# Performance work log

Measured on AMD Instinct MI355X. Metric: run time of the kernel, lower is better.

## Reference

```python
import jax, jax.numpy as jnp
import numpy as np

B, C, N, V, W = 2, 4, 224, 7, 256
EMB, H = 256, 4
TOKEN_DIM = C * N           # 896
HF = int(C * 2.66)          # 10 (GDFN hidden features)
EPS_LN = 1e-6


def _dwconv3(x, w):
    # depthwise 3x3, padding=1; x:[B,Ch,Hh,Ww], w:[Ch,1,3,3]
    return jax.lax.conv_general_dilated(
        x, w, window_strides=(1, 1), padding='SAME',
        feature_group_count=x.shape[1],
        dimension_numbers=('NCHW', 'OIHW', 'NCHW'))


def _layernorm_c(x, g, b):
    # LayerNorm over channel dim (NCHW), eps=1e-6
    m = jnp.mean(x, axis=1, keepdims=True)
    v = jnp.mean((x - m) ** 2, axis=1, keepdims=True)
    return (x - m) / jnp.sqrt(v + EPS_LN) * g[None, :, None, None] + b[None, :, None, None]


def setup_inputs() -> dict:
    key = jax.random.key(0)
    ks = jax.random.split(key, 12)
    s = 0.02
    return {
        'buffer':     jax.random.normal(ks[0], (B, C, N, V, W), jnp.float32),
        'w_in':       jax.random.normal(ks[1], (EMB, TOKEN_DIM), jnp.float32) * s,
        'temperature': jnp.ones((1, H, 1, 1), jnp.float32),
        'ln1_g':      jnp.ones((EMB,), jnp.float32),
        'ln1_b':      jnp.zeros((EMB,), jnp.float32),
        'w_qkv':      jax.random.normal(ks[2], (3 * EMB, EMB), jnp.float32) * s,
        'w_qkv_dw':   jax.random.normal(ks[3], (3 * EMB, 1, 3, 3), jnp.float32) * s,
        'w_proj':     jax.random.normal(ks[4], (TOKEN_DIM, EMB), jnp.float32) * s,
        'w_attca':    jax.random.normal(ks[5], (2 * H, H), jnp.float32) * s,
        'ln2_g':      jnp.ones((C,), jnp.float32),
        'ln2_b':      jnp.zeros((C,), jnp.float32),
        'w_pin':      jax.random.normal(ks[6], (2 * HF, C), jnp.float32) * s,
        'w_dw':       jax.random.normal(ks[7], (2 * HF, 1, 3, 3), jnp.float32) * s,
        'w_pout':     jax.random.normal(ks[8], (C, HF), jnp.float32) * s,
    }


def reference(buffer, w_in, temperature, ln1_g, ln1_b, w_qkv, w_qkv_dw,
              w_proj, w_attca, ln2_g, ln2_b, w_pin, w_dw, w_pout):
    S = V * W
    d = EMB // H
    # b c n v w -> b (v w) (c n)
    x_tok = buffer.transpose(0, 3, 4, 1, 2).reshape(B, S, C * N)
    # b c n v w -> (b n) c v w
    x_res = buffer.transpose(0, 2, 1, 3, 4).reshape(B * N, C, V, W)

    x_tok = jnp.einsum('bsk,ek->bse', x_tok, w_in)                  # linear_in
    x = x_tok.reshape(B, V, W, EMB).transpose(0, 3, 1, 2)           # b emb v w
    x_norm = _layernorm_c(x, ln1_g, ln1_b)

    qkv = jnp.einsum('bchw,oc->bohw', x_norm, w_qkv)                # 1x1 conv
    qkv = _dwconv3(qkv, w_qkv_dw)
    q, k, v_ = jnp.split(qkv, 3, axis=1)

    def heads(t):  # b (h d) v w -> b h (v w) d
        return t.reshape(B, H, d, S).transpose(0, 1, 3, 2)
    q, k, v_ = heads(q), heads(k), heads(v_)

    # F.normalize(dim=-1), eps=1e-12
    q = q / jnp.maximum(jnp.linalg.norm(q, axis=-1, keepdims=True), 1e-12)
    k = k / jnp.maximum(jnp.linalg.norm(k, axis=-1, keepdims=True), 1e-12)

    attn_logits = jnp.einsum('bhid,bhjd->bhij', q, k) * temperature
    attn0 = jax.nn.softmax(attn_logits, axis=-1)
    attn1 = jnp.maximum(attn_logits, 0.0) ** 2
    attn1 = jax.nn.gelu(attn1, approximate=False) * attn1
    x_att = jnp.einsum('bhij,oh->boij', attn1, w_attca)             # 1x1 conv over heads
    scale, shift = jnp.split(x_att, 2, axis=1)
    attn = attn0 * (1.0 + scale) + shift

    out = jnp.einsum('bhij,bhjd->bhid', attn, v_)
    out = out.transpose(0, 1, 3, 2).reshape(B, EMB, V, W)           # b (h d) v w
    out = jnp.einsum('bchw,oc->bohw', out, w_proj)                  # proj to token_dim
    out = out.reshape(B, C, N, V, W).transpose(0, 2, 1, 3, 4).reshape(B * N, C, V, W)

    x2 = x_res + out
    epi = _layernorm_c(x2, ln2_g, ln2_b)
    # GDFN
    h_ = jnp.einsum('bchw,oc->bohw', epi, w_pin)
    h_ = _dwconv3(h_, w_dw)
    h1, h2 = jnp.split(h_, 2, axis=1)
    h_ = jax.nn.gelu(h1, approximate=False) * h2
    epi = jnp.einsum('bchw,oc->bohw', h_, w_pout)
    epi = x2 + epi

    return epi.reshape(B, N, C, V, W).transpose(0, 2, 1, 3, 4)      # b c n v w
```

## Files before the change

kernel.cpp:

```cpp
#include <hip/hip_runtime.h>
#include <math.h>

#define B_ 2
#define C_ 4
#define N_ 224
#define V_ 7
#define W_ 256
#define S_ 1792
#define EMB_ 256
#define H_ 4
#define D_ 64
#define TOK_ 896
#define HF_ 10
#define JC_ 4
#define JRANGE_ (S_ / JC_)
#define JSTEPS_ (JRANGE_ / 32)

typedef __attribute__((ext_vector_type(8))) short short8;
typedef __attribute__((ext_vector_type(4))) float f32x4;

#define MFMA16(a, b, c) __builtin_amdgcn_mfma_f32_16x16x32_bf16(a, b, c, 0, 0, 0)

__device__ inline short f2bf(float f) {
    union { float f; unsigned u; } x; x.f = f;
    unsigned u = x.u;
    unsigned r = (u + 0x7fffu + ((u >> 16) & 1u)) >> 16;
    return (short)r;
}
__device__ inline float bf2f(short s) {
    union { unsigned u; float f; } x;
    x.u = ((unsigned)(unsigned short)s) << 16;
    return x.f;
}

template<bool COLSUM, bool LNB, bool BBF>
__global__ __launch_bounds__(256) void gemm_kernel(
    const float* __restrict__ A, const void* __restrict__ Bv, float* __restrict__ Cm,
    int M, int N, int K, long b_bs, long c_bs,
    const float* __restrict__ csin, float* __restrict__ csout,
    const float* __restrict__ lg, const float* __restrict__ lb)
{
    const int bz = blockIdx.z;
    Cm += (long)bz * c_bs;
    const int m0 = blockIdx.y * 64, n0 = blockIdx.x * 128;
    __shared__ __align__(16) short As[64 * 32];
    __shared__ __align__(16) short Bs[128 * 32];
    const int t = threadIdx.x;
    const int lane = t & 63, wave = t >> 6;
    const int wr = wave >> 1, wc = wave & 1;
    const int col = lane & 15, grp = lane >> 4;
    const int arow = t >> 2, akc = (t & 3) * 8;
    const int bn = t & 127, bkc = (t >> 7) * 16;
    float mean = 0.f, rstd = 1.f;
    if (LNB) {
        float s = 0.f, q = 0.f;
        #pragma unroll
        for (int mb = 0; mb < 4; ++mb) {
            s += csin[((long)(bz * 4 + mb) * 2 + 0) * N + n0 + bn];
            q += csin[((long)(bz * 4 + mb) * 2 + 1) * N + n0 + bn];
        }
        mean = s * (1.f / 256.f);
        rstd = rsqrtf(q * (1.f / 256.f) - mean * mean + 1e-6f);
    }
    f32x4 acc[2][4];
    #pragma unroll
    for (int i = 0; i < 2; ++i)
        #pragma unroll
        for (int j = 0; j < 4; ++j) acc[i][j] = (f32x4){0.f, 0.f, 0.f, 0.f};
    for (int k0 = 0; k0 < K; k0 += 32) {
        {
            const float* ap = &A[(long)(m0 + arow) * K + k0 + akc];
            f32x4 a0 = *(const f32x4*)ap;
            f32x4 a1 = *(const f32x4*)(ap + 4);
            short8 av;
            av[0] = f2bf(a0[0]); av[1] = f2bf(a0[1]); av[2] = f2bf(a0[2]); av[3] = f2bf(a0[3]);
            av[4] = f2bf(a1[0]); av[5] = f2bf(a1[1]); av[6] = f2bf(a1[2]); av[7] = f2bf(a1[3]);
            int abyte = (arow << 6) + (akc << 1);
            *(short8*)((char*)As + (abyte ^ ((arow & 7) << 4))) = av;
        }
        {
            short8 b0, b1;
            if (BBF) {
                const short* Bp = (const short*)Bv + (long)bz * b_bs;
                #pragma unroll
                for (int j = 0; j < 8; ++j) {
                    b0[j] = Bp[(long)(k0 + bkc + j) * N + n0 + bn];
                    b1[j] = Bp[(long)(k0 + bkc + 8 + j) * N + n0 + bn];
                }
            } else {
                const float* Bp = (const float*)Bv + (long)bz * b_bs;
                #pragma unroll
                for (int j = 0; j < 16; ++j) {
                    float v = Bp[(long)(k0 + bkc + j) * N + n0 + bn];
                    if (LNB) v = fmaf((v - mean) * rstd, lg[k0 + bkc + j], lb[k0 + bkc + j]);
                    if (j < 8) b0[j] = f2bf(v); else b1[j - 8] = f2bf(v);
                }
            }
            int bbyte = (bn << 6) + (bkc << 1);
            *(short8*)((char*)Bs + ((bbyte) ^ ((bn & 7) << 4))) = b0;
            *(short8*)((char*)Bs + ((bbyte + 16) ^ ((bn & 7) << 4))) = b1;
        }
        __syncthreads();
        short8 af[2], bfv[4];
        #pragma unroll
        for (int mm = 0; mm < 2; ++mm) {
            int r = wr * 32 + mm * 16 + col;
            af[mm] = *(const short8*)((const char*)As + (((r << 6) + (grp << 4)) ^ ((r & 7) << 4)));
        }
        #pragma unroll
        for (int nn = 0; nn < 4; ++nn) {
            int r = wc * 64 + nn * 16 + col;
            bfv[nn] = *(const short8*)((const char*)Bs + (((r << 6) + (grp << 4)) ^ ((r & 7) << 4)));
        }
        #pragma unroll
        for (int mm = 0; mm < 2; ++mm)
            #pragma unroll
            for (int nn = 0; nn < 4; ++nn)
                acc[mm][nn] = MFMA16(af[mm], bfv[nn], acc[mm][nn]);
        __syncthreads();
    }
    #pragma unroll
    for (int mm = 0; mm < 2; ++mm)
        #pragma unroll
        for (int nn = 0; nn < 4; ++nn)
            #pragma unroll
            for (int r = 0; r < 4; ++r)
                Cm[(long)(m0 + wr * 32 + mm * 16 + grp * 4 + r) * N
                   + n0 + wc * 64 + nn * 16 + col] = acc[mm][nn][r];
    if (COLSUM) {
        float* red = (float*)As;
        #pragma unroll
        for (int nn = 0; nn < 4; ++nn) {
            float s = 0.f, q = 0.f;
            #pragma unroll
            for (int mm = 0; mm < 2; ++mm)
                #pragma unroll
                for (int r = 0; r < 4; ++r) { float v = acc[mm][nn][r]; s += v; q += v * v; }
            s += __shfl_xor(s, 16, 64); s += __shfl_xor(s, 32, 64);
            q += __shfl_xor(q, 16, 64); q += __shfl_xor(q, 32, 64);
            if (lane < 16) {
                int cidx = wc * 64 + nn * 16 + col;
                red[(wr * 128 + cidx) * 2]     = s;
                red[(wr * 128 + cidx) * 2 + 1] = q;
            }
        }
        __syncthreads();
        if (wave < 2 && lane < 16) {
            #pragma unroll
            for (int nn = 0; nn < 4; ++nn) {
                int cidx = wc * 64 + nn * 16 + col;
                float s = red[cidx * 2]     + red[(128 + cidx) * 2];
                float q = red[cidx * 2 + 1] + red[(128 + cidx) * 2 + 1];
                csout[((long)(bz * 4 + blockIdx.y) * 2 + 0) * N + n0 + cidx] = s;
                csout[((long)(bz * 4 + blockIdx.y) * 2 + 1) * N + n0 + cidx] = q;
            }
        }
    }
}

__global__ void dwconv3_kernel(const float* __restrict__ X, const float* __restrict__ Wt,
                               float* __restrict__ Y, short* __restrict__ vbf,
                               long total, int Ch)
{
    long idx = (long)blockIdx.x * blockDim.x + threadIdx.x;
    long stride = (long)gridDim.x * blockDim.x;
    for (; idx < total; idx += stride) {
        int w = (int)(idx % W_);
        long t = idx / W_;
        int h = (int)(t % V_); t /= V_;
        int ch = (int)(t % Ch);
        long img_ch = idx / ((long)V_ * W_);
        const float* wp = Wt + ch * 9;
        const float* xp = X + img_ch * (V_ * W_);
        float acc = 0.f;
        #pragma unroll
        for (int dy = -1; dy <= 1; ++dy) {
            int h2 = h + dy;
            if (h2 < 0 || h2 >= V_) continue;
            #pragma unroll
            for (int dx = -1; dx <= 1; ++dx) {
                int w2 = w + dx;
                if (w2 < 0 || w2 >= W_) continue;
                acc += xp[h2 * W_ + w2] * wp[(dy + 1) * 3 + (dx + 1)];
            }
        }
        Y[idx] = acc;
        if (vbf && ch >= 512) {
            int b = (int)(t / Ch);
            vbf[((long)b * 256 + (ch - 512)) * S_ + h * W_ + w] = f2bf(acc);
        }
    }
}

__global__ __launch_bounds__(256) void headnorm_kernel(
    const float* __restrict__ qkvd, const float* __restrict__ temp,
    short* __restrict__ qn, short* __restrict__ kn)
{
    int s0 = blockIdx.x * 64;
    int bh = blockIdx.y; int b = bh >> 2, h = bh & 3;
    int isq = blockIdx.z;
    int ch0 = b * 768 + (isq ? 0 : EMB_) + h * 64;
    short* dst = (isq ? qn : kn) + (long)bh * S_ * 64;
    __shared__ float tile[64][65];
    __shared__ float red[64][4];
    int t = threadIdx.x;
    int sl = t & 63, dg = t >> 6;
    float part = 0.f;
    for (int dd = 0; dd < 16; ++dd) {
        int d = dg * 16 + dd;
        float v = qkvd[(long)(ch0 + d) * S_ + s0 + sl];
        tile[sl][d] = v;
        part += v * v;
    }
    red[sl][dg] = part;
    __syncthreads();
    int d = t & 63, sg = t >> 6;
    float tmul = isq ? temp[h] : 1.f;
    for (int si = 0; si < 16; ++si) {
        int s = sg * 16 + si;
        float nrm = sqrtf(red[s][0] + red[s][1] + red[s][2] + red[s][3]);
        float scale = tmul / fmaxf(nrm, 1e-12f);
        dst[(long)(s0 + s) * 64 + d] = f2bf(tile[s][d] * scale);
    }
}

__global__ __launch_bounds__(256) void attn_kernel(
    const short* __restrict__ qn, const short* __restrict__ kn,
    const short* __restrict__ vbf, const float* __restrict__ wat,
    short* __restrict__ partY, float* __restrict__ partZ)
{
    const int h = threadIdx.x >> 6;
    const int lane = threadIdx.x & 63;
    const int col = lane & 15, grp = lane >> 4;
    const int itile = blockIdx.x;
    const int jc = blockIdx.y;
    const int b = blockIdx.z;
    const int ibase = itile * 16;
    const int bh = b * 4 + h;

    const short* qrow = qn + ((long)bh * S_ + ibase + col) * 64 + grp * 8;
    short8 qa0 = *(const short8*)qrow;
    short8 qa1 = *(const short8*)(qrow + 32);
    float wsc[4], wsh[4];
    #pragma unroll
    for (int hh = 0; hh < 4; ++hh) { wsc[hh] = wat[h * 4 + hh]; wsh[hh] = wat[(4 + h) * 4 + hh]; }

    __shared__ __align__(16) float exch[2][4][16][36];

    f32x4 y1[4], y2[4];
    #pragma unroll
    for (int dt = 0; dt < 4; ++dt) {
        y1[dt] = (f32x4){0.f, 0.f, 0.f, 0.f};
        y2[dt] = (f32x4){0.f, 0.f, 0.f, 0.f};
    }
    float z = 0.f;
    const short* kbase = kn + (long)bh * S_ * 64;
    const short* vbase = vbf + ((long)b * 256 + h * 64) * S_;
    const int joffA = (col & 3) + 8 * (col >> 2);

    for (int jt = 0; jt < JSTEPS_; ++jt) {
        const int jbase = jc * JRANGE_ + jt * 32;
        const int buf = jt & 1;
        f32x4 lf[2];
        __builtin_amdgcn_s_setprio(1);
        #pragma unroll
        for (int tt = 0; tt < 2; ++tt) {
            const short* krow = kbase + (long)(jbase + joffA + 4 * tt) * 64 + grp * 8;
            short8 ka0 = *(const short8*)krow;
            short8 ka1 = *(const short8*)(krow + 32);
            f32x4 a = (f32x4){0.f, 0.f, 0.f, 0.f};
            a = MFMA16(ka0, qa0, a);
            a = MFMA16(ka1, qa1, a);
            lf[tt] = a;
        }
        __builtin_amdgcn_s_setprio(0);
        f32x4 a1v[2];
        float ee[2][4];
        #pragma unroll
        for (int tt = 0; tt < 2; ++tt) {
            #pragma unroll
            for (int r = 0; r < 4; ++r) {
                float l = lf[tt][r];
                float rr = fmaxf(l, 0.f);
                float s1 = rr * rr;
                float u = fmaf(s1 * s1, 0.0713548162726f * s1, 1.59576912161f * s1);
                float sg = __builtin_amdgcn_rcpf(1.f + __expf(-u));
                a1v[tt][r] = s1 * sg * s1;
                ee[tt][r] = __expf(l);
            }
            *(f32x4*)&exch[buf][h][col][8 * grp + 4 * tt] = a1v[tt];
        }
        __syncthreads();
        short8 pa, pb;
        #pragma unroll
        for (int tt = 0; tt < 2; ++tt) {
            f32x4 scv = a1v[tt] * wsc[h];
            f32x4 shv = a1v[tt] * wsh[h];
            #pragma unroll
            for (int hh = 0; hh < 4; ++hh) {
                if (hh == h) continue;
                f32x4 o = *(const f32x4*)&exch[buf][hh][col][8 * grp + 4 * tt];
                scv += o * wsc[hh];
                shv += o * wsh[hh];
            }
            #pragma unroll
            for (int r = 0; r < 4; ++r) {
                float e = ee[tt][r];
                z += e;
                pa[tt * 4 + r] = f2bf(e * (1.f + scv[r]));
                pb[tt * 4 + r] = f2bf(shv[r]);
            }
        }
        __builtin_amdgcn_s_setprio(1);
        #pragma unroll
        for (int dt = 0; dt < 4; ++dt) {
            const short* vrow = vbase + (long)(dt * 16 + col) * S_ + jbase + grp * 8;
            short8 vb = *(const short8*)vrow;
            y1[dt] = MFMA16(pa, vb, y1[dt]);
            y2[dt] = MFMA16(pb, vb, y2[dt]);
        }
        __builtin_amdgcn_s_setprio(0);
    }

    z += __shfl_xor(z, 16, 64);
    z += __shfl_xor(z, 32, 64);
    if (grp == 0)
        partZ[((long)(jc * 2 + b) * 4 + h) * S_ + ibase + col] = z;

    float* tb = &exch[0][h][0][0];
    long ybase = ((((long)jc * 2 + b) * 4 + h) * 2) * 64 * S_;
    for (int acc = 0; acc < 2; ++acc) {
        #pragma unroll
        for (int dt = 0; dt < 4; ++dt) {
            f32x4 y = acc ? y2[dt] : y1[dt];
            #pragma unroll
            for (int r = 0; r < 4; ++r) tb[(grp * 4 + r) * 17 + col] = y[r];
            #pragma unroll
            for (int p = 0; p < 4; ++p) {
                float val = tb[col * 17 + p * 4 + grp];
                partY[ybase + ((long)acc * 64 + dt * 16 + p * 4 + grp) * S_ + ibase + col] = f2bf(val);
            }
        }
    }
}

__global__ __launch_bounds__(256) void combine_kernel(
    const short* __restrict__ partY, const float* __restrict__ partZ,
    short* __restrict__ outav)
{
    int idx = blockIdx.x * 256 + threadIdx.x;
    int i = idx % S_;
    int t = idx / S_;
    int d = t & 63; t >>= 6;
    int h = t & 3; int b = t >> 2;
    float y1 = 0.f, y2 = 0.f, z = 0.f;
    #pragma unroll
    for (int jc = 0; jc < JC_; ++jc) {
        long base = ((((long)jc * 2 + b) * 4 + h) * 2) * 64 * S_;
        y1 += bf2f(partY[base + (long)d * S_ + i]);
        y2 += bf2f(partY[base + (long)(64 + d) * S_ + i]);
        z  += partZ[((long)(jc * 2 + b) * 4 + h) * S_ + i];
    }
    outav[((long)b * 256 + h * 64 + d) * S_ + i] = f2bf(y1 / z + y2);
}

__global__ __launch_bounds__(256) void resid_pin_kernel(
    const float* __restrict__ buffer, const float* __restrict__ proj,
    const float* __restrict__ g2, const float* __restrict__ b2,
    const float* __restrict__ w_pin,
    float* __restrict__ x2, short* __restrict__ hbuf)
{
    int s = blockIdx.x * 256 + threadIdx.x;
    int bn = blockIdx.y;
    int b = bn / N_, n = bn % N_;
    float v[4];
    float sum = 0.f;
    #pragma unroll
    for (int c = 0; c < 4; ++c) {
        float xr = buffer[((long)(b * 4 + c) * N_ + n) * S_ + s];
        float pr = proj[((long)b * TOK_ + c * N_ + n) * S_ + s];
        v[c] = xr + pr;
        x2[((long)bn * 4 + c) * S_ + s] = v[c];
        sum += v[c];
    }
    float mean = sum * 0.25f;
    float var = 0.f;
    #pragma unroll
    for (int c = 0; c < 4; ++c) { float dd = v[c] - mean; var += dd * dd; }
    var *= 0.25f;
    float inv = rsqrtf(var + 1e-6f);
    float e[4];
    #pragma unroll
    for (int c = 0; c < 4; ++c) e[c] = (v[c] - mean) * inv * g2[c] + b2[c];
    for (int o = 0; o < 2 * HF_; ++o) {
        float a = 0.f;
        #pragma unroll
        for (int c = 0; c < 4; ++c) a += w_pin[o * 4 + c] * e[c];
        hbuf[((long)bn * (2 * HF_) + o) * S_ + s] = f2bf(a);
    }
}

__global__ __launch_bounds__(448) void gdfn_kernel(
    const short* __restrict__ hbuf, const float* __restrict__ w_dw,
    const float* __restrict__ w_pout, const float* __restrict__ x2,
    float* __restrict__ out)
{
    int xt = blockIdx.x;
    int bn = blockIdx.y;
    int b = bn / N_, n = bn % N_;
    int x0 = xt * 64;
    __shared__ float tile[20][7][66];
    int tid = threadIdx.x;
    for (int idx = tid; idx < 20 * 7 * 66; idx += 448) {
        int ch = idx / (7 * 66); int rem = idx % (7 * 66);
        int y = rem / 66; int xx = rem % 66;
        int gx = x0 + xx - 1;
        float v = 0.f;
        if (gx >= 0 && gx < W_) v = bf2f(hbuf[((long)bn * 20 + ch) * S_ + y * W_ + gx]);
        tile[ch][y][xx] = v;
    }
    __syncthreads();
    int y = tid / 64, x = tid & 63;
    float hd[20];
    #pragma unroll
    for (int ch = 0; ch < 20; ++ch) {
        const float* wp = w_dw + ch * 9;
        float acc = 0.f;
        #pragma unroll
        for (int dy = -1; dy <= 1; ++dy) {
            int yy = y + dy;
            if (yy < 0 || yy >= V_) continue;
            #pragma unroll
            for (int dx = -1; dx <= 1; ++dx)
                acc += tile[ch][yy][x + 1 + dx] * wp[(dy + 1) * 3 + (dx + 1)];
        }
        hd[ch] = acc;
    }
    float g[HF_];
    #pragma unroll
    for (int f = 0; f < HF_; ++f) {
        float h1 = hd[f];
        g[f] = 0.5f * h1 * (1.f + erff(h1 * 0.70710678118654752f)) * hd[HF_ + f];
    }
    int s = y * W_ + x0 + x;
    #pragma unroll
    for (int c = 0; c < 4; ++c) {
        float a = 0.f;
        #pragma unroll
        for (int f = 0; f < HF_; ++f) a += w_pout[c * HF_ + f] * g[f];
        out[((long)(b * 4 + c) * N_ + n) * S_ + s] = x2[((long)bn * 4 + c) * S_ + s] + a;
    }
}

extern "C" void kernel_launch(void* const* d_in, const int* in_sizes, int n_in,
                              void* d_out, int out_size, void* d_ws, size_t ws_size,
                              hipStream_t stream)
{
    const float* buffer = (const float*)d_in[0];
    const float* w_in   = (const float*)d_in[1];
    const float* temp   = (const float*)d_in[2];
    const float* ln1_g  = (const float*)d_in[3];
    const float* ln1_b  = (const float*)d_in[4];
    const float* w_qkv  = (const float*)d_in[5];
    const float* w_qkv_dw = (const float*)d_in[6];
    const float* w_proj = (const float*)d_in[7];
    const float* w_attca = (const float*)d_in[8];
    const float* ln2_g  = (const float*)d_in[9];
    const float* ln2_b  = (const float*)d_in[10];
    const float* w_pin  = (const float*)d_in[11];
    const float* w_dw   = (const float*)d_in[12];
    const float* w_pout = (const float*)d_in[13];
    float* out = (float*)d_out;

    float* ws = (float*)d_ws;
    float* qkvd    = ws;
    short* qn      = (short*)(ws + 2752512);
    short* kn      = (short*)(ws + 3211264);
    short* vbf     = (short*)(ws + 3670016);
    short* partY   = (short*)(ws + 4128768);
    float* partZ   = ws + 7798784;
    short* outav   = (short*)(ws + 7856128);
    float* xw      = ws + 8314880;
    float* colsum  = ws + 9232384;
    float* qkv     = ws + 9261056;
    float* outproj = ws + 12013568;
    float* x2      = ws + 15224832;
    short* hbuf    = (short*)(ws + 18436096);

    gemm_kernel<true, false, false><<<dim3(14, 4, 2), 256, 0, stream>>>(
        w_in, buffer, xw, EMB_, S_, TOK_, (long)TOK_ * S_, (long)EMB_ * S_,
        nullptr, colsum, nullptr, nullptr);

    gemm_kernel<false, true, false><<<dim3(14, 12, 2), 256, 0, stream>>>(
        w_qkv, xw, qkv, 3 * EMB_, S_, EMB_, (long)EMB_ * S_, (long)3 * EMB_ * S_,
        colsum, nullptr, ln1_g, ln1_b);

    {
        long total = (long)B_ * 3 * EMB_ * S_;
        dwconv3_kernel<<<(int)((total + 255) / 256), 256, 0, stream>>>(
            qkv, w_qkv_dw, qkvd, vbf, total, 3 * EMB_);
    }

    headnorm_kernel<<<dim3(28, 8, 2), 256, 0, stream>>>(qkvd, temp, qn, kn);

    attn_kernel<<<dim3(112, JC_, B_), 256, 0, stream>>>(qn, kn, vbf, w_attca, partY, partZ);

    combine_kernel<<<3584, 256, 0, stream>>>(partY, partZ, outav);

    gemm_kernel<false, false, true><<<dim3(14, 14, 2), 256, 0, stream>>>(
        w_proj, outav, outproj, TOK_, S_, EMB_, (long)EMB_ * S_, (long)TOK_ * S_,
        nullptr, nullptr, nullptr, nullptr);

    resid_pin_kernel<<<dim3(7, B_ * N_), 256, 0, stream>>>(
        buffer, outproj, ln2_g, ln2_b, w_pin, x2, hbuf);

    gdfn_kernel<<<dim3(4, B_ * N_), 448, 0, stream>>>(hbuf, w_dw, w_pout, x2, out);
}
```

Baseline: 217.2 us.

## Split attention key range into eight chunks and restructure head-mixing exchange

Doubles the number of key-range chunks in the attention kernel, so the grid has twice as many blocks and each does half the key steps. The head-mixing exchange moves from a double-buffered vectorized layout to a single transposed padded buffer with an extra barrier per step, and the s_setprio hints are removed. Workspace offsets grow to hold twice the partial outputs. The combine stage now has to read more partials, and the extra barrier adds synchronization cost.

```diff
diff --git a/kernel.cpp b/kernel.cpp
--- a/kernel.cpp
+++ b/kernel.cpp
@@ -12,7 +12,7 @@
 #define D_ 64
 #define TOK_ 896
 #define HF_ 10
-#define JC_ 4
+#define JC_ 8
 #define JRANGE_ (S_ / JC_)
 #define JSTEPS_ (JRANGE_ / 32)
 
@@ -245,7 +245,7 @@
     #pragma unroll
     for (int hh = 0; hh < 4; ++hh) { wsc[hh] = wat[h * 4 + hh]; wsh[hh] = wat[(4 + h) * 4 + hh]; }
 
-    __shared__ __align__(16) float exch[2][4][16][36];
+    __shared__ float exch[4][32][34];
 
     f32x4 y1[4], y2[4];
     #pragma unroll
@@ -259,10 +259,8 @@
     const int joffA = (col & 3) + 8 * (col >> 2);
 
     for (int jt = 0; jt < JSTEPS_; ++jt) {
-        const int jbase = jc * JRANGE_ + jt * 32;
-        const int buf = jt & 1;
+        int jbase = jc * JRANGE_ + jt * 32;
         f32x4 lf[2];
-        __builtin_amdgcn_s_setprio(1);
         #pragma unroll
         for (int tt = 0; tt < 2; ++tt) {
             const short* krow = kbase + (long)(jbase + joffA + 4 * tt) * 64 + grp * 8;
@@ -273,11 +271,9 @@
             a = MFMA16(ka1, qa1, a);
             lf[tt] = a;
         }
-        __builtin_amdgcn_s_setprio(0);
-        f32x4 a1v[2];
-        float ee[2][4];
-        #pragma unroll
-        for (int tt = 0; tt < 2; ++tt) {
+        float a1own[2][4], ee[2][4];
+        #pragma unroll
+        for (int tt = 0; tt < 2; ++tt)
             #pragma unroll
             for (int r = 0; r < 4; ++r) {
                 float l = lf[tt][r];
@@ -285,33 +281,31 @@
                 float s1 = rr * rr;
                 float u = fmaf(s1 * s1, 0.0713548162726f * s1, 1.59576912161f * s1);
                 float sg = __builtin_amdgcn_rcpf(1.f + __expf(-u));
-                a1v[tt][r] = s1 * sg * s1;
+                float a1 = s1 * sg * s1;
+                a1own[tt][r] = a1;
                 ee[tt][r] = __expf(l);
-            }
-            *(f32x4*)&exch[buf][h][col][8 * grp + 4 * tt] = a1v[tt];
-        }
+                exch[h][r + 4 * tt + 8 * grp][col] = a1;
+            }
         __syncthreads();
         short8 pa, pb;
         #pragma unroll
-        for (int tt = 0; tt < 2; ++tt) {
-            f32x4 scv = a1v[tt] * wsc[h];
-            f32x4 shv = a1v[tt] * wsh[h];
-            #pragma unroll
-            for (int hh = 0; hh < 4; ++hh) {
-                if (hh == h) continue;
-                f32x4 o = *(const f32x4*)&exch[buf][hh][col][8 * grp + 4 * tt];
-                scv += o * wsc[hh];
-                shv += o * wsh[hh];
-            }
+        for (int tt = 0; tt < 2; ++tt)
             #pragma unroll
             for (int r = 0; r < 4; ++r) {
+                int jloc = r + 4 * tt + 8 * grp;
+                float sc = 0.f, sh = 0.f;
+                #pragma unroll
+                for (int hh = 0; hh < 4; ++hh) {
+                    float a1v = (hh == h) ? a1own[tt][r] : exch[hh][jloc][col];
+                    sc += a1v * wsc[hh];
+                    sh += a1v * wsh[hh];
+                }
                 float e = ee[tt][r];
                 z += e;
-                pa[tt * 4 + r] = f2bf(e * (1.f + scv[r]));
-                pb[tt * 4 + r] = f2bf(shv[r]);
-            }
-        }
-        __builtin_amdgcn_s_setprio(1);
+                pa[tt * 4 + r] = f2bf(e * (1.f + sc));
+                pb[tt * 4 + r] = f2bf(sh);
+            }
+        __syncthreads();
         #pragma unroll
         for (int dt = 0; dt < 4; ++dt) {
             const short* vrow = vbase + (long)(dt * 16 + col) * S_ + jbase + grp * 8;
@@ -319,7 +313,6 @@
             y1[dt] = MFMA16(pa, vb, y1[dt]);
             y2[dt] = MFMA16(pb, vb, y2[dt]);
         }
-        __builtin_amdgcn_s_setprio(0);
     }
 
     z += __shfl_xor(z, 16, 64);
@@ -327,7 +320,8 @@
     if (grp == 0)
         partZ[((long)(jc * 2 + b) * 4 + h) * S_ + ibase + col] = z;
 
-    float* tb = &exch[0][h][0][0];
+    __syncthreads();
+    float* tb = &exch[h][0][0];
     long ybase = ((((long)jc * 2 + b) * 4 + h) * 2) * 64 * S_;
     for (int acc = 0; acc < 2; ++acc) {
         #pragma unroll
@@ -478,14 +472,14 @@
     short* kn      = (short*)(ws + 3211264);
     short* vbf     = (short*)(ws + 3670016);
     short* partY   = (short*)(ws + 4128768);
-    float* partZ   = ws + 7798784;
-    short* outav   = (short*)(ws + 7856128);
-    float* xw      = ws + 8314880;
-    float* colsum  = ws + 9232384;
-    float* qkv     = ws + 9261056;
-    float* outproj = ws + 12013568;
-    float* x2      = ws + 15224832;
-    short* hbuf    = (short*)(ws + 18436096);
+    float* partZ   = ws + 18808832;
+    short* outav   = (short*)(ws + 18923520);
+    float* xw      = ws + 19382272;
+    float* colsum  = ws + 20299776;
+    float* qkv     = ws + 20328448;
+    float* outproj = ws + 23080960;
+    float* x2      = ws + 26292224;
+    short* hbuf    = (short*)(ws + 29503488);
 
     gemm_kernel<true, false, false><<<dim3(14, 4, 2), 256, 0, stream>>>(
         w_in, buffer, xw, EMB_, S_, TOK_, (long)TOK_ * S_, (long)EMB_ * S_,
```

Result: faster. 197.6 us (-9.0%).
